# Performance work log

Hardware: AMD Instinct MI355X
Metric: run time of the kernel (lower is better)

Reference implementation:

```python
import jax, jax.numpy as jnp
import numpy as np

B, S, D, H = 2, 2048, 1024, 16
HD = D // H  # 64


def setup_inputs() -> dict:
    key = jax.random.key(0)
    ks = jax.random.split(key, 10)
    q = jax.random.normal(ks[0], (B, S, D), dtype=jnp.float32)
    k = jax.random.normal(ks[1], (B, S, D), dtype=jnp.float32)
    v = jax.random.normal(ks[2], (B, S, D), dtype=jnp.float32)
    # additive mask: 1 where attention is disallowed (causal), broadcast over B,H
    mask = (1.0 - jnp.tril(jnp.ones((S, S), dtype=jnp.float32)))[None, None, :, :]
    sc = 1.0 / np.sqrt(D)
    Wk = jax.random.normal(ks[3], (D, D), dtype=jnp.float32) * sc
    bk = jnp.zeros((D,), dtype=jnp.float32)
    Wv = jax.random.normal(ks[4], (D, D), dtype=jnp.float32) * sc
    bv = jnp.zeros((D,), dtype=jnp.float32)
    Wo = jax.random.normal(ks[5], (D, D), dtype=jnp.float32) * sc
    bo = jnp.zeros((D,), dtype=jnp.float32)
    return {"q": q, "k": k, "v": v, "mask": mask,
            "Wk": Wk, "bk": bk, "Wv": Wv, "bv": bv, "Wo": Wo, "bo": bo}


def _split_heads(x):
    b, s, d = x.shape
    return x.reshape(b, s, H, HD).transpose(0, 2, 1, 3)  # [B,H,S,HD]


def reference(q, k, v, mask, Wk, bk, Wv, bv, Wo, bo):
    # NOTE: source bug reproduced — q is projected with Wk (wq is unused).
    _q = _split_heads(q @ Wk + bk)
    _k = _split_heads(k @ Wk + bk)
    _v = _split_heads(v @ Wv + bv)
    scale = jnp.sqrt(jnp.float32(HD)) + 1e-8
    score = jnp.einsum('bhqd,bhkd->bhqk', _q, _k) / scale
    score = score + mask * (-1e9)
    attn = jax.nn.softmax(score, axis=-1)
    o = jnp.einsum('bhqk,bhkd->bhqd', attn, _v)
    o = o.transpose(0, 2, 1, 3).reshape(q.shape[0], q.shape[1], -1)  # [B,S,D]
    # dropout is identity at inference (training=False)
    return o @ Wo + bo
```

## Files before the change

### kernel.cpp

```cpp
#include <hip/hip_runtime.h>


#define Bn 2
#define Sn 2048
#define Dn 1024
#define Hn 16
#define HDn 64

typedef short bs8 __attribute__((ext_vector_type(8)));
typedef float f32x4 __attribute__((ext_vector_type(4)));
typedef unsigned int u32;
typedef unsigned int u32x2 __attribute__((ext_vector_type(2)));

__device__ __forceinline__ short f2bf(float f) {
    u32 x = __builtin_bit_cast(u32, f);
    x = x + 0x7fffu + ((x >> 16) & 1u);
    return (short)(x >> 16);
}
__device__ __forceinline__ u32 cvtpk(float lo, float hi) {
    u32 r;
    asm("v_cvt_pk_bf16_f32 %0, %1, %2" : "=v"(r) : "v"(lo), "v"(hi));
    return r;
}
__device__ __forceinline__ void gload16(const void* g, void* l) {
    __builtin_amdgcn_global_load_lds(
        (const __attribute__((address_space(1))) u32*)g,
        (__attribute__((address_space(3))) u32*)l, 16, 0, 0);
}

__global__ __launch_bounds__(256) void cvt_qkv(const float* __restrict__ q,
                                               const float* __restrict__ k,
                                               const float* __restrict__ v,
                                               short* __restrict__ out) {
    int z = blockIdx.y;
    const float* in = z == 0 ? q : z == 1 ? k : v;
    short* o = out + (size_t)z * (Bn * Sn * Dn);
    int i = blockIdx.x * 256 + threadIdx.x;
    const f32x4* p = reinterpret_cast<const f32x4*>(in) + (size_t)i * 2;
    f32x4 a = p[0], b = p[1];
    bs8 ov;
    ov[0]=f2bf(a[0]); ov[1]=f2bf(a[1]); ov[2]=f2bf(a[2]); ov[3]=f2bf(a[3]);
    ov[4]=f2bf(b[0]); ov[5]=f2bf(b[1]); ov[6]=f2bf(b[2]); ov[7]=f2bf(b[3]);
    reinterpret_cast<bs8*>(o)[i] = ov;
}

__global__ __launch_bounds__(256) void cvt_w(const float* __restrict__ Wk,
                                             const float* __restrict__ Wv,
                                             const float* __restrict__ Wo,
                                             short* __restrict__ Wt) {
    __shared__ float tile[32][33];
    int z = blockIdx.z;
    const float* W = z == 0 ? Wk : z == 1 ? Wv : Wo;
    short* o = Wt + (size_t)z * Dn * Dn;
    int tx = threadIdx.x & 31;
    int ty = threadIdx.x >> 5;
    int bi = blockIdx.y * 32;
    int bo = blockIdx.x * 32;
    #pragma unroll
    for (int k2 = 0; k2 < 4; k2++)
        tile[ty + k2*8][tx] = W[(size_t)(bi + ty + k2*8) * Dn + bo + tx];
    __syncthreads();
    #pragma unroll
    for (int k2 = 0; k2 < 4; k2++)
        o[(size_t)(bo + ty + k2*8) * Dn + bi + tx] = f2bf(tile[tx][ty + k2*8]);
}

__global__ __launch_bounds__(256) void proj3(const short* __restrict__ qb,
                                             const short* __restrict__ kb,
                                             const short* __restrict__ vb,
                                             const short* __restrict__ Wall,
                                             const float* __restrict__ bk,
                                             const float* __restrict__ bv,
                                             short* __restrict__ Qp,
                                             short* __restrict__ Kp,
                                             short* __restrict__ Vtp) {
    constexpr int K = Dn;
    __shared__ __align__(16) short As[128 * 32];
    __shared__ __align__(16) short Bs[128 * 32];
    int z = blockIdx.z;
    const short* A  = z == 0 ? qb : z == 1 ? kb : vb;
    const short* Bt = z == 2 ? Wall + (1 << 20) : Wall;
    const float* bias = z == 2 ? bv : bk;
    int tid = threadIdx.x;
    int m0 = blockIdx.x * 128, n0 = blockIdx.y * 128;
    int w = tid >> 6, lane = tid & 63;
    int wr = (w >> 1) * 64, wc = (w & 1) * 64;
    int fr = lane & 15, fq = lane >> 4;
    f32x4 acc[4][4] = {};
    const short* Ag  = A  + (size_t)(m0 + (tid >> 2)) * K + (tid & 3) * 8;
    const short* Ag2 = Ag + (size_t)64 * K;
    const short* Bg  = Bt + (size_t)(n0 + (tid >> 2)) * K + (tid & 3) * 8;
    const short* Bg2 = Bg + (size_t)64 * K;
    short* AsL = As + tid * 8;
    short* BsL = Bs + tid * 8;

    for (int k0 = 0; k0 < K; k0 += 32) {
        gload16(Ag + k0, AsL);
        gload16(Ag2 + k0, AsL + 2048);
        gload16(Bg + k0, BsL);
        gload16(Bg2 + k0, BsL + 2048);
        __syncthreads();
        bs8 af[4], bfv[4];
        #pragma unroll
        for (int i = 0; i < 4; i++)
            af[i] = *reinterpret_cast<const bs8*>(&As[(wr + i*16 + fr) * 32 + fq * 8]);
        #pragma unroll
        for (int j = 0; j < 4; j++)
            bfv[j] = *reinterpret_cast<const bs8*>(&Bs[(wc + j*16 + fr) * 32 + fq * 8]);
        #pragma unroll
        for (int i = 0; i < 4; i++)
            #pragma unroll
            for (int j = 0; j < 4; j++)
                acc[i][j] = __builtin_amdgcn_mfma_f32_16x16x32_bf16(af[i], bfv[j], acc[i][j], 0, 0, 0);
        __syncthreads();
    }

    if (z == 2) {
        #pragma unroll
        for (int j = 0; j < 4; j++) {
            int col = n0 + wc + j*16 + fr;
            float bvv = bias[col];
            #pragma unroll
            for (int i = 0; i < 4; i++) {
                int row0 = m0 + wr + i*16 + fq*4;
                int bb = row0 >> 11, s0 = row0 & (Sn - 1);
                size_t base = (size_t)bb * (Dn * Sn) + (size_t)col * Sn + s0;
                u32x2 pv;
                pv[0] = cvtpk(acc[i][j][0] + bvv, acc[i][j][1] + bvv);
                pv[1] = cvtpk(acc[i][j][2] + bvv, acc[i][j][3] + bvv);
                *reinterpret_cast<u32x2*>(&Vtp[base]) = pv;
            }
        }
    } else {
        float sc = (z == 0) ? 0.18033688011112042f : 1.0f;
        short* outp = (z == 0) ? Qp : Kp;
        #pragma unroll
        for (int j = 0; j < 4; j++) {
            int col = n0 + wc + j*16 + fr;
            float bvv = bias[col];
            #pragma unroll
            for (int i = 0; i < 4; i++) {
                int row0 = m0 + wr + i*16 + fq*4;
                #pragma unroll
                for (int r = 0; r < 4; r++)
                    outp[(size_t)(row0 + r) * Dn + col] = f2bf((acc[i][j][r] + bvv) * sc);
            }
        }
    }
}

__global__ __launch_bounds__(256) void gemm_out(const short* __restrict__ A,
                                                const short* __restrict__ Bt,
                                                const float* __restrict__ bias,
                                                float* __restrict__ Cout) {
    constexpr int K = Dn, N = Dn;
    __shared__ __align__(16) short As[64][32];
    __shared__ __align__(16) short Bs[128][32];
    int tid = threadIdx.x;
    int m0 = blockIdx.x * 64, n0 = blockIdx.y * 128;
    int w = tid >> 6, lane = tid & 63;
    int wr = (w >> 1) * 32, wc = (w & 1) * 64;
    int fr = lane & 15, fq = lane >> 4;
    f32x4 acc[2][4] = {};
    const short* Ag  = A  + (size_t)(m0 + (tid >> 2)) * K + (tid & 3) * 8;
    const short* Bg0 = Bt + (size_t)(n0 + (tid >> 2)) * K + (tid & 3) * 8;
    const short* Bg1 = Bg0 + (size_t)64 * K;
    short* AsL  = &As[0][0] + tid * 8;
    short* BsL0 = &Bs[0][0] + tid * 8;
    short* BsL1 = BsL0 + 2048;

    for (int k0 = 0; k0 < K; k0 += 32) {
        gload16(Ag + k0, AsL);
        gload16(Bg0 + k0, BsL0);
        gload16(Bg1 + k0, BsL1);
        __syncthreads();
        bs8 af[2], bfv[4];
        #pragma unroll
        for (int i = 0; i < 2; i++)
            af[i] = *reinterpret_cast<const bs8*>(&As[wr + i*16 + fr][fq*8]);
        #pragma unroll
        for (int j = 0; j < 4; j++)
            bfv[j] = *reinterpret_cast<const bs8*>(&Bs[wc + j*16 + fr][fq*8]);
        #pragma unroll
        for (int i = 0; i < 2; i++)
            #pragma unroll
            for (int j = 0; j < 4; j++)
                acc[i][j] = __builtin_amdgcn_mfma_f32_16x16x32_bf16(af[i], bfv[j], acc[i][j], 0, 0, 0);
        __syncthreads();
    }
    #pragma unroll
    for (int j = 0; j < 4; j++) {
        int col = n0 + wc + j*16 + fr;
        float bv = bias[col];
        #pragma unroll
        for (int i = 0; i < 2; i++) {
            int row0 = m0 + wr + i*16 + fq*4;
            #pragma unroll
            for (int r = 0; r < 4; r++)
                Cout[(size_t)(row0 + r) * N + col] = acc[i][j][r] + bv;
        }
    }
}

__global__ __launch_bounds__(256) void attn_fwd(const short* __restrict__ Qp,
                                                const short* __restrict__ Kp,
                                                const short* __restrict__ Vt,
                                                short* __restrict__ O) {
    __shared__ __align__(16) char Kb[64 * 128];
    __shared__ __align__(16) char Vb[64 * 128];
    __shared__ __align__(16) u32  Pw[4][16][36];
    __shared__ __align__(16) short Ot[4][16][72];
    int qt = 31 - (int)blockIdx.x;
    int bh = blockIdx.y, bb = bh >> 4, h = bh & 15;
    int tid = threadIdx.x, w = tid >> 6, lane = tid & 63;
    int fr = lane & 15, fq = lane >> 4;
    int wloc = w * 16 + fr;
    int q0 = qt * 64 + w * 16;

    const short* Qg = Qp + (size_t)(bb * Sn + q0 + fr) * Dn + h * HDn + fq * 8;
    bs8 qf0 = *reinterpret_cast<const bs8*>(Qg);
    bs8 qf1 = *reinterpret_cast<const bs8*>(Qg + 32);

    f32x4 oacc[4] = {};
    float m_run = -3e38f, l_run = 0.f;

    int sr = tid >> 2, scB = (tid & 3) * 32, swz = (sr & 7) << 4;
    int wofs0 = sr * 128 + (scB ^ swz);
    int wofs1 = sr * 128 + ((scB + 16) ^ swz);
    const short* Kg = Kp + (size_t)(bb * Sn + sr) * Dn + h * HDn + (tid & 3) * 16;
    const short* Vg = Vt + (size_t)bb * (Dn * Sn) + (size_t)(h * HDn + sr) * Sn + (tid & 3) * 16;

    int rs = (fr & 7) << 4;
    int rb0 = (fq * 16) ^ rs;
    int rb1 = (64 + fq * 16) ^ rs;
    u32* PwL = &Pw[w][fr][0];
    u32* PwS = PwL + 2 * fq;

    for (int kt = 0; kt <= qt; kt++) {
        int kv0 = kt * 64;
        bs8 k0v = *reinterpret_cast<const bs8*>(Kg + (size_t)kv0 * Dn);
        bs8 k1v = *reinterpret_cast<const bs8*>(Kg + (size_t)kv0 * Dn + 8);
        bs8 v0v = *reinterpret_cast<const bs8*>(Vg + kv0);
        bs8 v1v = *reinterpret_cast<const bs8*>(Vg + kv0 + 8);
        __syncthreads();
        *reinterpret_cast<bs8*>(Kb + wofs0) = k0v;
        *reinterpret_cast<bs8*>(Kb + wofs1) = k1v;
        *reinterpret_cast<bs8*>(Vb + wofs0) = v0v;
        *reinterpret_cast<bs8*>(Vb + wofs1) = v1v;
        __syncthreads();

        float p[4][4];
        #pragma unroll
        for (int n = 0; n < 4; n++) {
            const char* Krow = Kb + (n * 16 + fr) * 128;
            bs8 kf0 = *reinterpret_cast<const bs8*>(Krow + rb0);
            bs8 kf1 = *reinterpret_cast<const bs8*>(Krow + rb1);
            f32x4 t = {};
            t = __builtin_amdgcn_mfma_f32_16x16x32_bf16(kf0, qf0, t, 0, 0, 0);
            t = __builtin_amdgcn_mfma_f32_16x16x32_bf16(kf1, qf1, t, 0, 0, 0);
            p[n][0] = t[0]; p[n][1] = t[1]; p[n][2] = t[2]; p[n][3] = t[3];
        }
        if (kt == qt) {
            #pragma unroll
            for (int n = 0; n < 4; n++)
                #pragma unroll
                for (int r = 0; r < 4; r++)
                    if (n * 16 + fq * 4 + r > wloc) p[n][r] = -1.8e8f;
        }

        float m01 = fmaxf(fmaxf(p[0][0], p[0][1]), fmaxf(p[0][2], p[0][3]));
        float m23 = fmaxf(fmaxf(p[1][0], p[1][1]), fmaxf(p[1][2], p[1][3]));
        float m45 = fmaxf(fmaxf(p[2][0], p[2][1]), fmaxf(p[2][2], p[2][3]));
        float m67 = fmaxf(fmaxf(p[3][0], p[3][1]), fmaxf(p[3][2], p[3][3]));
        float mloc = fmaxf(fmaxf(m01, m23), fmaxf(m45, m67));
        mloc = fmaxf(mloc, __shfl_xor(mloc, 16));
        mloc = fmaxf(mloc, __shfl_xor(mloc, 32));
        if (!__all(mloc <= m_run + 8.0f)) {
            float mn = fmaxf(m_run, mloc);
            float fac = exp2f(m_run - mn);
            m_run = mn;
            l_run *= fac;
            oacc[0] *= fac; oacc[1] *= fac; oacc[2] *= fac; oacc[3] *= fac;
        }
        float ssum = 0.f;
        #pragma unroll
        for (int n = 0; n < 4; n++)
            #pragma unroll
            for (int r = 0; r < 4; r++) {
                float e = exp2f(p[n][r] - m_run);
                p[n][r] = e; ssum += e;
            }
        l_run += ssum;

        #pragma unroll
        for (int n = 0; n < 4; n++) {
            u32x2 pr;
            pr[0] = cvtpk(p[n][0], p[n][1]);
            pr[1] = cvtpk(p[n][2], p[n][3]);
            *reinterpret_cast<u32x2*>(PwS + 8 * n) = pr;
        }
        __builtin_amdgcn_wave_barrier();
        bs8 pf0 = *reinterpret_cast<const bs8*>(PwL + 4 * fq);
        bs8 pf1 = *reinterpret_cast<const bs8*>(PwL + 16 + 4 * fq);

        #pragma unroll
        for (int n = 0; n < 4; n++) {
            const char* Vrow = Vb + (n * 16 + fr) * 128;
            bs8 vf0 = *reinterpret_cast<const bs8*>(Vrow + rb0);
            bs8 vf1 = *reinterpret_cast<const bs8*>(Vrow + rb1);
            oacc[n] = __builtin_amdgcn_mfma_f32_16x16x32_bf16(vf0, pf0, oacc[n], 0, 0, 0);
            oacc[n] = __builtin_amdgcn_mfma_f32_16x16x32_bf16(vf1, pf1, oacc[n], 0, 0, 0);
        }
    }

    l_run += __shfl_xor(l_run, 16);
    l_run += __shfl_xor(l_run, 32);
    float inv = 1.f / l_run;
    #pragma unroll
    for (int n = 0; n < 4; n++) {
        u32x2 ov;
        ov[0] = cvtpk(oacc[n][0] * inv, oacc[n][1] * inv);
        ov[1] = cvtpk(oacc[n][2] * inv, oacc[n][3] * inv);
        *reinterpret_cast<u32x2*>(&Ot[w][fr][n * 16 + fq * 4]) = ov;
    }
    __builtin_amdgcn_wave_barrier();
    bs8 o0 = *reinterpret_cast<const bs8*>(&Ot[w][fr][fq * 16]);
    bs8 o1 = *reinterpret_cast<const bs8*>(&Ot[w][fr][fq * 16 + 8]);
    short* Og = O + (size_t)(bb * Sn + q0 + fr) * Dn + h * HDn + fq * 16;
    *reinterpret_cast<bs8*>(Og) = o0;
    *reinterpret_cast<bs8*>(Og + 8) = o1;
}

extern "C" void kernel_launch(void* const* d_in, const int* in_sizes, int n_in,
                              void* d_out, int out_size, void* d_ws, size_t ws_size,
                              hipStream_t stream) {
    const float* q  = (const float*)d_in[0];
    const float* k  = (const float*)d_in[1];
    const float* v  = (const float*)d_in[2];
    const float* Wk = (const float*)d_in[4];
    const float* bk = (const float*)d_in[5];
    const float* Wv = (const float*)d_in[6];
    const float* bv = (const float*)d_in[7];
    const float* Wo = (const float*)d_in[8];
    const float* bo = (const float*)d_in[9];

    char* ws = (char*)d_ws;
    const size_t MB = (size_t)1 << 20;
    short* Wall = (short*)ws;
    short* Wot  = Wall + 2 * (1 << 20);
    short* qb   = (short*)(ws + 6*MB);
    short* kb   = (short*)(ws + 14*MB);
    short* vb   = (short*)(ws + 22*MB);
    short* Qp   = (short*)(ws + 30*MB);
    short* Kp   = (short*)(ws + 38*MB);
    short* Vtp  = (short*)(ws + 46*MB);
    short* Oa   = qb;

    cvt_qkv<<<dim3(2048, 3), dim3(256), 0, stream>>>(q, k, v, qb);
    cvt_w<<<dim3(32, 32, 3), dim3(256), 0, stream>>>(Wk, Wv, Wo, Wall);

    proj3<<<dim3(32, 8, 3), dim3(256), 0, stream>>>(qb, kb, vb, Wall, bk, bv, Qp, Kp, Vtp);

    attn_fwd<<<dim3(32, 32), dim3(256), 0, stream>>>(Qp, Kp, Vtp, Oa);

    gemm_out<<<dim3(64, 8), dim3(256), 0, stream>>>(Oa, Wot, bo, (float*)d_out);
}
```

Before: 261.0 us.

## Rewrite attention with 32x32 MFMA, 128-row query tiles and register-resident P

The attention kernel now uses 32x32x16 bf16 MFMA with each wave owning 32 query rows, so a block covers 128 queries and the grid halves. The P matrix is rearranged into B-operand layout in registers with permlane32 swaps instead of a round trip through LDS. K/V tiles are loaded straight into LDS with global_load_lds. Waves skip fully masked KV tiles. The aim is fewer LDS round trips and more MFMA work per tile. The cost is higher register pressure and fewer blocks for the GPU to spread across its compute units.

Measured after the change: 262.4 us. Within noise of the previous version (+0.5%).

```diff
diff --git a/kernel.cpp b/kernel.cpp
--- a/kernel.cpp
+++ b/kernel.cpp
@@ -9,8 +9,10 @@
 
 typedef short bs8 __attribute__((ext_vector_type(8)));
 typedef float f32x4 __attribute__((ext_vector_type(4)));
+typedef float f32x16 __attribute__((ext_vector_type(16)));
 typedef unsigned int u32;
 typedef unsigned int u32x2 __attribute__((ext_vector_type(2)));
+typedef unsigned int u32x4 __attribute__((ext_vector_type(4)));
 
 __device__ __forceinline__ short f2bf(float f) {
     u32 x = __builtin_bit_cast(u32, f);
@@ -22,6 +24,11 @@
     asm("v_cvt_pk_bf16_f32 %0, %1, %2" : "=v"(r) : "v"(lo), "v"(hi));
     return r;
 }
+__device__ __forceinline__ u32x2 pl32swap(u32 a, u32 b) {
+    return __builtin_amdgcn_permlane32_swap(a, b, false, false);
+}
+__device__ __forceinline__ float asf(u32 x) { return __builtin_bit_cast(float, x); }
+__device__ __forceinline__ u32 asu(float x) { return __builtin_bit_cast(u32, x); }
 __device__ __forceinline__ void gload16(const void* g, void* l) {
     __builtin_amdgcn_global_load_lds(
         (const __attribute__((address_space(1))) u32*)g,
@@ -208,127 +215,147 @@
                                                 short* __restrict__ O) {
     __shared__ __align__(16) char Kb[64 * 128];
     __shared__ __align__(16) char Vb[64 * 128];
-    __shared__ __align__(16) u32  Pw[4][16][36];
-    __shared__ __align__(16) short Ot[4][16][72];
-    int qt = 31 - (int)blockIdx.x;
+    __shared__ __align__(16) u32 Ot[4][32 * 36];
+    int qt = 15 - (int)blockIdx.x;
     int bh = blockIdx.y, bb = bh >> 4, h = bh & 15;
     int tid = threadIdx.x, w = tid >> 6, lane = tid & 63;
-    int fr = lane & 15, fq = lane >> 4;
-    int wloc = w * 16 + fr;
-    int q0 = qt * 64 + w * 16;
-
-    const short* Qg = Qp + (size_t)(bb * Sn + q0 + fr) * Dn + h * HDn + fq * 8;
-    bs8 qf0 = *reinterpret_cast<const bs8*>(Qg);
-    bs8 qf1 = *reinterpret_cast<const bs8*>(Qg + 32);
-
-    f32x4 oacc[4] = {};
+    int lq = lane & 31, hi = lane >> 5;
+    int q0 = qt * 128 + w * 32;
+    int qg = q0 + lq;
+    int qw_end = q0 + 31;
+
+    const short* Qrow = Qp + (size_t)(bb * Sn + qg) * Dn + h * HDn;
+    bs8 qf[4];
+    #pragma unroll
+    for (int t = 0; t < 4; t++)
+        qf[t] = *reinterpret_cast<const bs8*>(Qrow + 16 * t + 8 * hi);
+
+    f32x16 oacc0 = {}, oacc1 = {};
     float m_run = -3e38f, l_run = 0.f;
 
-    int sr = tid >> 2, scB = (tid & 3) * 32, swz = (sr & 7) << 4;
-    int wofs0 = sr * 128 + (scB ^ swz);
-    int wofs1 = sr * 128 + ((scB + 16) ^ swz);
-    const short* Kg = Kp + (size_t)(bb * Sn + sr) * Dn + h * HDn + (tid & 3) * 16;
-    const short* Vg = Vt + (size_t)bb * (Dn * Sn) + (size_t)(h * HDn + sr) * Sn + (tid & 3) * 16;
-
-    int rs = (fr & 7) << 4;
-    int rb0 = (fq * 16) ^ rs;
-    int rb1 = (64 + fq * 16) ^ rs;
-    u32* PwL = &Pw[w][fr][0];
-    u32* PwS = PwL + 2 * fq;
-
-    for (int kt = 0; kt <= qt; kt++) {
+    int srow = 16 * w + (lane >> 3);
+    int scol = (8 * (lane & 7)) ^ ((lane >> 3) << 3);
+    const short* KgB = Kp + (size_t)(bb * Sn + srow) * Dn + h * HDn + scol;
+    const short* VgB = Vt + (size_t)bb * (Dn * Sn) + (size_t)(h * HDn + srow) * Sn + scol;
+    char* KdA = Kb + (16 * w) * 128;
+    char* KdB = KdA + 8 * 128;
+    char* VdA = Vb + (16 * w) * 128;
+    char* VdB = VdA + 8 * 128;
+
+    int rsw = (lq & 7) << 4;
+    const char* Krow0 = Kb + lq * 128;
+    const char* Krow1 = Kb + (32 + lq) * 128;
+    const char* Vrow0 = Vb + lq * 128;
+    const char* Vrow1 = Vb + (32 + lq) * 128;
+
+    int nkv = 2 * qt + 2;
+    for (int kt = 0; kt < nkv; kt++) {
         int kv0 = kt * 64;
-        bs8 k0v = *reinterpret_cast<const bs8*>(Kg + (size_t)kv0 * Dn);
-        bs8 k1v = *reinterpret_cast<const bs8*>(Kg + (size_t)kv0 * Dn + 8);
-        bs8 v0v = *reinterpret_cast<const bs8*>(Vg + kv0);
-        bs8 v1v = *reinterpret_cast<const bs8*>(Vg + kv0 + 8);
-        __syncthreads();
-        *reinterpret_cast<bs8*>(Kb + wofs0) = k0v;
-        *reinterpret_cast<bs8*>(Kb + wofs1) = k1v;
-        *reinterpret_cast<bs8*>(Vb + wofs0) = v0v;
-        *reinterpret_cast<bs8*>(Vb + wofs1) = v1v;
-        __syncthreads();
-
-        float p[4][4];
-        #pragma unroll
-        for (int n = 0; n < 4; n++) {
-            const char* Krow = Kb + (n * 16 + fr) * 128;
-            bs8 kf0 = *reinterpret_cast<const bs8*>(Krow + rb0);
-            bs8 kf1 = *reinterpret_cast<const bs8*>(Krow + rb1);
-            f32x4 t = {};
-            t = __builtin_amdgcn_mfma_f32_16x16x32_bf16(kf0, qf0, t, 0, 0, 0);
-            t = __builtin_amdgcn_mfma_f32_16x16x32_bf16(kf1, qf1, t, 0, 0, 0);
-            p[n][0] = t[0]; p[n][1] = t[1]; p[n][2] = t[2]; p[n][3] = t[3];
-        }
-        if (kt == qt) {
-            #pragma unroll
-            for (int n = 0; n < 4; n++)
-                #pragma unroll
-                for (int r = 0; r < 4; r++)
-                    if (n * 16 + fq * 4 + r > wloc) p[n][r] = -1.8e8f;
-        }
-
-        float m01 = fmaxf(fmaxf(p[0][0], p[0][1]), fmaxf(p[0][2], p[0][3]));
-        float m23 = fmaxf(fmaxf(p[1][0], p[1][1]), fmaxf(p[1][2], p[1][3]));
-        float m45 = fmaxf(fmaxf(p[2][0], p[2][1]), fmaxf(p[2][2], p[2][3]));
-        float m67 = fmaxf(fmaxf(p[3][0], p[3][1]), fmaxf(p[3][2], p[3][3]));
-        float mloc = fmaxf(fmaxf(m01, m23), fmaxf(m45, m67));
-        mloc = fmaxf(mloc, __shfl_xor(mloc, 16));
-        mloc = fmaxf(mloc, __shfl_xor(mloc, 32));
+        __syncthreads();
+        gload16(KgB + (size_t)kv0 * Dn, KdA);
+        gload16(KgB + (size_t)kv0 * Dn + 8 * Dn, KdB);
+        gload16(VgB + kv0, VdA);
+        gload16(VgB + kv0 + 8 * Sn, VdB);
+        __syncthreads();
+        if (kv0 > qw_end) continue;
+
+        f32x16 s0 = {}, s1 = {};
+        #pragma unroll
+        for (int t = 0; t < 4; t++) {
+            int ofs = (32 * t + 16 * hi) ^ rsw;
+            bs8 kf0 = *reinterpret_cast<const bs8*>(Krow0 + ofs);
+            bs8 kf1 = *reinterpret_cast<const bs8*>(Krow1 + ofs);
+            s0 = __builtin_amdgcn_mfma_f32_32x32x16_bf16(kf0, qf[t], s0, 0, 0, 0);
+            s1 = __builtin_amdgcn_mfma_f32_32x32x16_bf16(kf1, qf[t], s1, 0, 0, 0);
+        }
+        if (kv0 + 63 > q0) {
+            #pragma unroll
+            for (int r = 0; r < 16; r++) {
+                int c = (r & 3) + 8 * (r >> 2) + 4 * hi;
+                if (kv0 + c > qg)      s0[r] = -1.8e8f;
+                if (kv0 + 32 + c > qg) s1[r] = -1.8e8f;
+            }
+        }
+
+        float mloc = fmaxf(s0[0], s1[0]);
+        #pragma unroll
+        for (int r = 1; r < 16; r++) mloc = fmaxf(mloc, fmaxf(s0[r], s1[r]));
+        {
+            u32x2 rr = pl32swap(asu(mloc), asu(mloc));
+            mloc = fmaxf(asf(rr[0]), asf(rr[1]));
+        }
         if (!__all(mloc <= m_run + 8.0f)) {
             float mn = fmaxf(m_run, mloc);
             float fac = exp2f(m_run - mn);
-            m_run = mn;
-            l_run *= fac;
-            oacc[0] *= fac; oacc[1] *= fac; oacc[2] *= fac; oacc[3] *= fac;
-        }
-        float ssum = 0.f;
-        #pragma unroll
-        for (int n = 0; n < 4; n++)
-            #pragma unroll
-            for (int r = 0; r < 4; r++) {
-                float e = exp2f(p[n][r] - m_run);
-                p[n][r] = e; ssum += e;
-            }
-        l_run += ssum;
-
-        #pragma unroll
-        for (int n = 0; n < 4; n++) {
-            u32x2 pr;
-            pr[0] = cvtpk(p[n][0], p[n][1]);
-            pr[1] = cvtpk(p[n][2], p[n][3]);
-            *reinterpret_cast<u32x2*>(PwS + 8 * n) = pr;
-        }
-        __builtin_amdgcn_wave_barrier();
-        bs8 pf0 = *reinterpret_cast<const bs8*>(PwL + 4 * fq);
-        bs8 pf1 = *reinterpret_cast<const bs8*>(PwL + 16 + 4 * fq);
-
-        #pragma unroll
-        for (int n = 0; n < 4; n++) {
-            const char* Vrow = Vb + (n * 16 + fr) * 128;
-            bs8 vf0 = *reinterpret_cast<const bs8*>(Vrow + rb0);
-            bs8 vf1 = *reinterpret_cast<const bs8*>(Vrow + rb1);
-            oacc[n] = __builtin_amdgcn_mfma_f32_16x16x32_bf16(vf0, pf0, oacc[n], 0, 0, 0);
-            oacc[n] = __builtin_amdgcn_mfma_f32_16x16x32_bf16(vf1, pf1, oacc[n], 0, 0, 0);
-        }
-    }
-
-    l_run += __shfl_xor(l_run, 16);
-    l_run += __shfl_xor(l_run, 32);
+            m_run = mn; l_run *= fac;
+            oacc0 *= fac; oacc1 *= fac;
+        }
+        float ss = 0.f;
+        #pragma unroll
+        for (int r = 0; r < 16; r++) {
+            s0[r] = exp2f(s0[r] - m_run); ss += s0[r];
+            s1[r] = exp2f(s1[r] - m_run); ss += s1[r];
+        }
+        l_run += ss;
+
+        u32 W0[8], W1[8];
+        #pragma unroll
+        for (int u = 0; u < 8; u++) {
+            W0[u] = cvtpk(s0[2*u], s0[2*u+1]);
+            W1[u] = cvtpk(s1[2*u], s1[2*u+1]);
+        }
+        u32x4 Bf[4];
+        #pragma unroll
+        for (int t = 0; t < 4; t++) {
+            int u0 = 4 * (t & 1);
+            u32 a0 = (t < 2) ? W0[u0]     : W1[u0];
+            u32 b0 = (t < 2) ? W0[u0 + 2] : W1[u0 + 2];
+            u32 a1 = (t < 2) ? W0[u0 + 1] : W1[u0 + 1];
+            u32 b1 = (t < 2) ? W0[u0 + 3] : W1[u0 + 3];
+            u32x2 r0 = pl32swap(a0, b0);
+            u32x2 r1 = pl32swap(a1, b1);
+            Bf[t][0] = r0[0]; Bf[t][1] = r1[0]; Bf[t][2] = r0[1]; Bf[t][3] = r1[1];
+        }
+
+        #pragma unroll
+        for (int t = 0; t < 4; t++) {
+            bs8 pB = __builtin_bit_cast(bs8, Bf[t]);
+            int ofs = (32 * t + 16 * hi) ^ rsw;
+            bs8 vf0 = *reinterpret_cast<const bs8*>(Vrow0 + ofs);
+            bs8 vf1 = *reinterpret_cast<const bs8*>(Vrow1 + ofs);
+            oacc0 = __builtin_amdgcn_mfma_f32_32x32x16_bf16(vf0, pB, oacc0, 0, 0, 0);
+            oacc1 = __builtin_amdgcn_mfma_f32_32x32x16_bf16(vf1, pB, oacc1, 0, 0, 0);
+        }
+    }
+
+    {
+        u32x2 rr = pl32swap(asu(l_run), asu(l_run));
+        l_run = asf(rr[0]) + asf(rr[1]);
+    }
     float inv = 1.f / l_run;
-    #pragma unroll
-    for (int n = 0; n < 4; n++) {
-        u32x2 ov;
-        ov[0] = cvtpk(oacc[n][0] * inv, oacc[n][1] * inv);
-        ov[1] = cvtpk(oacc[n][2] * inv, oacc[n][3] * inv);
-        *reinterpret_cast<u32x2*>(&Ot[w][fr][n * 16 + fq * 4]) = ov;
+
+    u32* OtW = Ot[w];
+    #pragma unroll
+    for (int m = 0; m < 2; m++) {
+        f32x16 oo = m ? oacc1 : oacc0;
+        #pragma unroll
+        for (int u = 0; u < 8; u += 2) {
+            u32x2 wv;
+            wv[0] = cvtpk(oo[2*u] * inv,     oo[2*u+1] * inv);
+            wv[1] = cvtpk(oo[2*u+2] * inv,   oo[2*u+3] * inv);
+            int widx = 16 * m + 4 * (u >> 1) + 2 * hi;
+            *reinterpret_cast<u32x2*>(OtW + lq * 36 + widx) = wv;
+        }
     }
     __builtin_amdgcn_wave_barrier();
-    bs8 o0 = *reinterpret_cast<const bs8*>(&Ot[w][fr][fq * 16]);
-    bs8 o1 = *reinterpret_cast<const bs8*>(&Ot[w][fr][fq * 16 + 8]);
-    short* Og = O + (size_t)(bb * Sn + q0 + fr) * Dn + h * HDn + fq * 16;
-    *reinterpret_cast<bs8*>(Og) = o0;
-    *reinterpret_cast<bs8*>(Og + 8) = o1;
+    int q2 = lane >> 1, hh = lane & 1;
+    const u32* rp = OtW + q2 * 36 + hh * 16;
+    short* Og = O + (size_t)(bb * Sn + q0 + q2) * Dn + h * HDn + hh * 32;
+    #pragma unroll
+    for (int c = 0; c < 4; c++) {
+        u32x4 vv = *reinterpret_cast<const u32x4*>(rp + 4 * c);
+        *reinterpret_cast<u32x4*>(Og + 8 * c) = vv;
+    }
 }
 
 extern "C" void kernel_launch(void* const* d_in, const int* in_sizes, int n_in,
@@ -361,7 +388,7 @@
 
     proj3<<<dim3(32, 8, 3), dim3(256), 0, stream>>>(qb, kb, vb, Wall, bk, bv, Qp, Kp, Vtp);
 
-    attn_fwd<<<dim3(32, 32), dim3(256), 0, stream>>>(Qp, Kp, Vtp, Oa);
+    attn_fwd<<<dim3(16, 32), dim3(256), 0, stream>>>(Qp, Kp, Vtp, Oa);
 
     gemm_out<<<dim3(64, 8), dim3(256), 0, stream>>>(Oa, Wot, bo, (float*)d_out);
 }
```
